# Optimization experiments

Hardware: AMD Instinct MI355X
Metric: run time of the kernel (lower is better)

## Reference

```python
import jax, jax.numpy as jnp
import numpy as np

B, C, H, W, D = 16, 512, 14, 14, 8000  # batch, channels(=input_dim1=input_dim2), spatial, output_dim


def _sketch_matrix(seed_h, seed_s, input_dim, output_dim):
    # Reproduce the module's count-sketch matrix generation (np.random.seed based).
    np.random.seed(seed_h)
    rand_h = np.random.randint(output_dim, size=input_dim)
    np.random.seed(seed_s)
    rand_s = (2 * np.random.randint(2, size=input_dim) - 1).astype(np.float32)
    M = np.zeros((input_dim, output_dim), dtype=np.float32)
    M[np.arange(input_dim), rand_h] = rand_s  # one-hot-per-row with sign
    return jnp.asarray(M)


def setup_inputs() -> dict:
    key = jax.random.key(0)
    x = jax.random.normal(key, (B, C, H, W), dtype=jnp.float32)
    S1 = _sketch_matrix(1, 3, C, D)
    S2 = _sketch_matrix(5, 7, C, D)
    return {"x": x, "S1": S1, "S2": S2}


def reference(x, S1, S2):
    b, c, h, w = x.shape
    # NCHW -> (B*H*W, C)
    flat = jnp.transpose(x, (0, 2, 3, 1)).reshape(-1, c)
    sketch1 = flat @ S1  # [BHW, D]
    sketch2 = flat @ S2  # [BHW, D]
    # circular convolution of the two count-sketches via FFT
    f1 = jnp.fft.fft(sketch1, axis=-1)
    f2 = jnp.fft.fft(sketch2, axis=-1)
    cbp_flat = jnp.fft.ifft(f1 * f2, axis=-1).real.astype(x.dtype)
    cbp = cbp_flat.reshape(b, h, w, -1)
    # sum_pool=True: reduce over spatial dims -> [B, D]
    return cbp.sum(axis=(1, 2))
```

## Files before the change

### kernel.cpp

```cpp
#include <hip/hip_runtime.h>

#define B_DIM 16
#define C_DIM 512
#define HW_DIM 196
#define D_DIM 8000
#define KP 224
#define NROW (B_DIM * C_DIM)

typedef __attribute__((ext_vector_type(8))) short short8;
typedef __attribute__((ext_vector_type(4))) float float4v;

__global__ __launch_bounds__(256) void prep(
    const float* __restrict__ x, const float* __restrict__ S1,
    const float* __restrict__ S2,
    int* __restrict__ h, float* __restrict__ s,
    unsigned short* __restrict__ xp) {
    const int bid = blockIdx.x;
    const int tid = threadIdx.x;
    if (bid < 512) {
        __shared__ int found;
        for (int rr = 0; rr < 2; ++rr) {
            const int r     = bid * 2 + rr;
            const int row   = r & (C_DIM - 1);
            const int which = r >> 9;
            const float4* rowp = (const float4*)((which ? S2 : S1) + (size_t)row * D_DIM);
            int*   hp = h + which * C_DIM;
            float* sp = s + which * C_DIM;
            if (tid == 0) found = 0;
            __syncthreads();
            for (int c = 0; c < 8; ++c) {
                int j4 = c * 256 + tid;
                if (j4 < D_DIM / 4) {
                    float4 v = rowp[j4];
                    if (v.x != 0.f) { hp[row] = 4 * j4 + 0; sp[row] = v.x; found = 1; }
                    if (v.y != 0.f) { hp[row] = 4 * j4 + 1; sp[row] = v.y; found = 1; }
                    if (v.z != 0.f) { hp[row] = 4 * j4 + 2; sp[row] = v.z; found = 1; }
                    if (v.w != 0.f) { hp[row] = 4 * j4 + 3; sp[row] = v.w; found = 1; }
                }
                __syncthreads();
                if (found) break;
            }
            __syncthreads();
        }
    } else {
        const int j = bid - 512;
        #pragma unroll
        for (int l = 0; l < 14; ++l) {
            int idx = l * 256 + tid;
            int r   = idx / KP;
            int kk  = idx - r * KP;
            int row = j * 16 + r;
            float v = (kk < HW_DIM) ? x[(size_t)row * HW_DIM + kk] : 0.0f;
            unsigned int u = __float_as_uint(v);
            u = (u + 0x7FFFu + ((u >> 16) & 1u)) >> 16;
            xp[(size_t)row * KP + kk] = (unsigned short)u;
        }
    }
}

__global__ __launch_bounds__(256) void gram_hist(
    const unsigned short* __restrict__ xp,
    const int* __restrict__ h, const float* __restrict__ s,
    float* __restrict__ part) {
    const int jb = blockIdx.x;
    const int ib = blockIdx.y;
    const int b  = blockIdx.z;
    const int i0 = ib * 128;
    const int j0 = jb * 64;
    const int tid = threadIdx.x;

    __shared__ __align__(16) float hist[D_DIM];

    #pragma unroll
    for (int l4 = 0; l4 < 7; ++l4)
        ((float4*)hist)[l4 * 256 + tid] = (float4){0.f, 0.f, 0.f, 0.f};
    if (tid < 2000 - 1792)
        ((float4*)hist)[1792 + tid] = (float4){0.f, 0.f, 0.f, 0.f};
    __syncthreads();

    const int w  = tid >> 6;
    const int l  = tid & 63;
    const int rA = l & 15;
    const int g  = l >> 4;

    const unsigned short* base = xp + (size_t)b * C_DIM * KP;
    const unsigned short* pA[2];
    const unsigned short* pB[4];
    #pragma unroll
    for (int mt = 0; mt < 2; ++mt)
        pA[mt] = base + (size_t)(i0 + w * 32 + mt * 16 + rA) * KP + g * 8;
    #pragma unroll
    for (int nt = 0; nt < 4; ++nt)
        pB[nt] = base + (size_t)(j0 + nt * 16 + rA) * KP + g * 8;

    float4v acc[2][4];
    #pragma unroll
    for (int mt = 0; mt < 2; ++mt)
        #pragma unroll
        for (int nt = 0; nt < 4; ++nt)
            acc[mt][nt] = (float4v){0.0f, 0.0f, 0.0f, 0.0f};

    short8 fa[2], fb[4];
    #pragma unroll
    for (int mt = 0; mt < 2; ++mt) fa[mt] = *(const short8*)pA[mt];
    #pragma unroll
    for (int nt = 0; nt < 4; ++nt) fb[nt] = *(const short8*)pB[nt];

    #pragma unroll
    for (int step = 1; step <= 7; ++step) {
        short8 na[2], nb[4];
        if (step < 7) {
            #pragma unroll
            for (int mt = 0; mt < 2; ++mt) na[mt] = *(const short8*)(pA[mt] + step * 32);
            #pragma unroll
            for (int nt = 0; nt < 4; ++nt) nb[nt] = *(const short8*)(pB[nt] + step * 32);
        }
        #pragma unroll
        for (int mt = 0; mt < 2; ++mt)
            #pragma unroll
            for (int nt = 0; nt < 4; ++nt)
                acc[mt][nt] = __builtin_amdgcn_mfma_f32_16x16x32_bf16(
                    fa[mt], fb[nt], acc[mt][nt], 0, 0, 0);
        if (step < 7) {
            #pragma unroll
            for (int mt = 0; mt < 2; ++mt) fa[mt] = na[mt];
            #pragma unroll
            for (int nt = 0; nt < 4; ++nt) fb[nt] = nb[nt];
        }
    }

    int hr[2][4]; float sr[2][4]; int hc[4]; float sc[4];
    #pragma unroll
    for (int mt = 0; mt < 2; ++mt)
        #pragma unroll
        for (int rg = 0; rg < 4; ++rg) {
            int c1 = i0 + w * 32 + mt * 16 + (l >> 4) * 4 + rg;
            hr[mt][rg] = h[c1]; sr[mt][rg] = s[c1];
        }
    #pragma unroll
    for (int nt = 0; nt < 4; ++nt) {
        int c2 = j0 + nt * 16 + (l & 15);
        hc[nt] = h[C_DIM + c2]; sc[nt] = s[C_DIM + c2];
    }
    #pragma unroll
    for (int mt = 0; mt < 2; ++mt)
        #pragma unroll
        for (int nt = 0; nt < 4; ++nt)
            #pragma unroll
            for (int rg = 0; rg < 4; ++rg) {
                int bin = hr[mt][rg] + hc[nt];
                if (bin >= D_DIM) bin -= D_DIM;
                atomicAdd(&hist[bin], sr[mt][rg] * sc[nt] * acc[mt][nt][rg]);
            }
    __syncthreads();

    const int slot = b * 32 + ib * 8 + jb;
    float* pb = part + (size_t)slot * D_DIM;
    #pragma unroll
    for (int l4 = 0; l4 < 7; ++l4)
        ((float4*)pb)[l4 * 256 + tid] = ((const float4*)hist)[l4 * 256 + tid];
    if (tid < 2000 - 1792)
        ((float4*)pb)[1792 + tid] = ((const float4*)hist)[1792 + tid];
}

__global__ __launch_bounds__(256) void reduce_part(
    const float* __restrict__ part, float* __restrict__ out) {
    int i4 = blockIdx.x * 256 + threadIdx.x;
    if (i4 >= B_DIM * D_DIM / 4) return;
    int b = i4 / (D_DIM / 4);
    int d = i4 - b * (D_DIM / 4);
    const float4* p = (const float4*)(part + (size_t)b * 32 * D_DIM) + d;
    float4 v = {0.f, 0.f, 0.f, 0.f};
    #pragma unroll
    for (int t = 0; t < 32; ++t) {
        float4 q = p[(size_t)t * (D_DIM / 4)];
        v.x += q.x; v.y += q.y; v.z += q.z; v.w += q.w;
    }
    ((float4*)out)[i4] = v;
}

extern "C" void kernel_launch(void* const* d_in, const int* in_sizes, int n_in,
                              void* d_out, int out_size, void* d_ws, size_t ws_size,
                              hipStream_t stream) {
    const float* x  = (const float*)d_in[0];
    const float* S1 = (const float*)d_in[1];
    const float* S2 = (const float*)d_in[2];
    float* out = (float*)d_out;

    int*            h    = (int*)d_ws;
    float*          s    = (float*)(h + 2 * C_DIM);
    unsigned short* xp   = (unsigned short*)(s + 2 * C_DIM);
    float*          part = (float*)(xp + (size_t)NROW * KP);

    prep<<<1024, 256, 0, stream>>>(x, S1, S2, h, s, xp);

    dim3 grid(8, 4, B_DIM);
    gram_hist<<<grid, 256, 0, stream>>>(xp, h, s, part);

    reduce_part<<<(B_DIM * D_DIM / 4 + 255) / 256, 256, 0, stream>>>(part, out);
}
```

Measured before the change: 117.1 us.

## Merge gram tiles into larger blocks and drop the partial-reduction kernel

Each gram_hist block now has 1024 threads and covers one quarter of a batch's rows, with every wave handling two output tiles. All tiles of a block share one LDS histogram, so there are 4 partial histograms per batch instead of 32. Those are atomically added straight into the output, which prep now zeroes, and the separate reduce kernel and its partial buffer go away. This cuts the partial-buffer memory traffic and one launch, but leaves only 64 blocks, which may underuse the GPU's compute units. It also adds global float atomics, so the summation order is no longer deterministic.

Result: slower. 177.5 us (+51.6%).

```diff
diff --git a/kernel.cpp b/kernel.cpp
--- a/kernel.cpp
+++ b/kernel.cpp
@@ -14,7 +14,7 @@
     const float* __restrict__ x, const float* __restrict__ S1,
     const float* __restrict__ S2,
     int* __restrict__ h, float* __restrict__ s,
-    unsigned short* __restrict__ xp) {
+    unsigned short* __restrict__ xp, float* __restrict__ out) {
     const int bid = blockIdx.x;
     const int tid = threadIdx.x;
     if (bid < 512) {
@@ -44,6 +44,8 @@
         }
     } else {
         const int j = bid - 512;
+        if (j < 125)
+            ((float4*)out)[j * 256 + tid] = (float4){0.f, 0.f, 0.f, 0.f};
         #pragma unroll
         for (int l = 0; l < 14; ++l) {
             int idx = l * 256 + tid;
@@ -58,24 +60,21 @@
     }
 }
 
-__global__ __launch_bounds__(256) void gram_hist(
+__global__ __launch_bounds__(1024, 4) void gram_hist(
     const unsigned short* __restrict__ xp,
     const int* __restrict__ h, const float* __restrict__ s,
-    float* __restrict__ part) {
-    const int jb = blockIdx.x;
-    const int ib = blockIdx.y;
-    const int b  = blockIdx.z;
-    const int i0 = ib * 128;
-    const int j0 = jb * 64;
+    float* __restrict__ out) {
+    const int b = blockIdx.x >> 2;
+    const int q = blockIdx.x & 3;
     const int tid = threadIdx.x;
 
     __shared__ __align__(16) float hist[D_DIM];
-
     #pragma unroll
-    for (int l4 = 0; l4 < 7; ++l4)
-        ((float4*)hist)[l4 * 256 + tid] = (float4){0.f, 0.f, 0.f, 0.f};
-    if (tid < 2000 - 1792)
-        ((float4*)hist)[1792 + tid] = (float4){0.f, 0.f, 0.f, 0.f};
+    for (int l4 = 0; l4 < 2; ++l4) {
+        int i4 = l4 * 1024 + tid;
+        if (i4 < D_DIM / 4)
+            ((float4*)hist)[i4] = (float4){0.f, 0.f, 0.f, 0.f};
+    }
     __syncthreads();
 
     const int w  = tid >> 6;
@@ -84,99 +83,92 @@
     const int g  = l >> 4;
 
     const unsigned short* base = xp + (size_t)b * C_DIM * KP;
-    const unsigned short* pA[2];
-    const unsigned short* pB[4];
+
     #pragma unroll
-    for (int mt = 0; mt < 2; ++mt)
-        pA[mt] = base + (size_t)(i0 + w * 32 + mt * 16 + rA) * KP + g * 8;
-    #pragma unroll
-    for (int nt = 0; nt < 4; ++nt)
-        pB[nt] = base + (size_t)(j0 + nt * 16 + rA) * KP + g * 8;
+    for (int pass = 0; pass < 2; ++pass) {
+        const int t  = w + pass * 16;
+        const int it = t & 3;
+        const int jt = t >> 2;
+        const int i0 = q * 128 + it * 32;
+        const int j0 = jt * 64;
 
-    float4v acc[2][4];
-    #pragma unroll
-    for (int mt = 0; mt < 2; ++mt)
+        const unsigned short* pA[2];
+        const unsigned short* pB[4];
+        #pragma unroll
+        for (int mt = 0; mt < 2; ++mt)
+            pA[mt] = base + (size_t)(i0 + mt * 16 + rA) * KP + g * 8;
         #pragma unroll
         for (int nt = 0; nt < 4; ++nt)
-            acc[mt][nt] = (float4v){0.0f, 0.0f, 0.0f, 0.0f};
+            pB[nt] = base + (size_t)(j0 + nt * 16 + rA) * KP + g * 8;
 
-    short8 fa[2], fb[4];
-    #pragma unroll
-    for (int mt = 0; mt < 2; ++mt) fa[mt] = *(const short8*)pA[mt];
-    #pragma unroll
-    for (int nt = 0; nt < 4; ++nt) fb[nt] = *(const short8*)pB[nt];
+        float4v acc[2][4];
+        #pragma unroll
+        for (int mt = 0; mt < 2; ++mt)
+            #pragma unroll
+            for (int nt = 0; nt < 4; ++nt)
+                acc[mt][nt] = (float4v){0.0f, 0.0f, 0.0f, 0.0f};
 
-    #pragma unroll
-    for (int step = 1; step <= 7; ++step) {
-        short8 na[2], nb[4];
-        if (step < 7) {
+        short8 fa[2], fb[4];
+        #pragma unroll
+        for (int mt = 0; mt < 2; ++mt) fa[mt] = *(const short8*)pA[mt];
+        #pragma unroll
+        for (int nt = 0; nt < 4; ++nt) fb[nt] = *(const short8*)pB[nt];
+
+        #pragma unroll
+        for (int step = 1; step <= 7; ++step) {
+            short8 na[2], nb[4];
+            if (step < 7) {
+                #pragma unroll
+                for (int mt = 0; mt < 2; ++mt) na[mt] = *(const short8*)(pA[mt] + step * 32);
+                #pragma unroll
+                for (int nt = 0; nt < 4; ++nt) nb[nt] = *(const short8*)(pB[nt] + step * 32);
+            }
             #pragma unroll
-            for (int mt = 0; mt < 2; ++mt) na[mt] = *(const short8*)(pA[mt] + step * 32);
+            for (int mt = 0; mt < 2; ++mt)
+                #pragma unroll
+                for (int nt = 0; nt < 4; ++nt)
+                    acc[mt][nt] = __builtin_amdgcn_mfma_f32_16x16x32_bf16(
+                        fa[mt], fb[nt], acc[mt][nt], 0, 0, 0);
+            if (step < 7) {
+                #pragma unroll
+                for (int mt = 0; mt < 2; ++mt) fa[mt] = na[mt];
+                #pragma unroll
+                for (int nt = 0; nt < 4; ++nt) fb[nt] = nb[nt];
+            }
+        }
+
+        int hr[2][4]; float sr[2][4]; int hc[4]; float sc[4];
+        #pragma unroll
+        for (int mt = 0; mt < 2; ++mt)
             #pragma unroll
-            for (int nt = 0; nt < 4; ++nt) nb[nt] = *(const short8*)(pB[nt] + step * 32);
+            for (int rg = 0; rg < 4; ++rg) {
+                int c1 = i0 + mt * 16 + (l >> 4) * 4 + rg;
+                hr[mt][rg] = h[c1]; sr[mt][rg] = s[c1];
+            }
+        #pragma unroll
+        for (int nt = 0; nt < 4; ++nt) {
+            int c2 = j0 + nt * 16 + (l & 15);
+            hc[nt] = h[C_DIM + c2]; sc[nt] = s[C_DIM + c2];
         }
         #pragma unroll
         for (int mt = 0; mt < 2; ++mt)
             #pragma unroll
             for (int nt = 0; nt < 4; ++nt)
-                acc[mt][nt] = __builtin_amdgcn_mfma_f32_16x16x32_bf16(
-                    fa[mt], fb[nt], acc[mt][nt], 0, 0, 0);
-        if (step < 7) {
-            #pragma unroll
-            for (int mt = 0; mt < 2; ++mt) fa[mt] = na[mt];
-            #pragma unroll
-            for (int nt = 0; nt < 4; ++nt) fb[nt] = nb[nt];
-        }
+                #pragma unroll
+                for (int rg = 0; rg < 4; ++rg) {
+                    int bin = hr[mt][rg] + hc[nt];
+                    if (bin >= D_DIM) bin -= D_DIM;
+                    atomicAdd(&hist[bin], sr[mt][rg] * sc[nt] * acc[mt][nt][rg]);
+                }
     }
-
-    int hr[2][4]; float sr[2][4]; int hc[4]; float sc[4];
-    #pragma unroll
-    for (int mt = 0; mt < 2; ++mt)
-        #pragma unroll
-        for (int rg = 0; rg < 4; ++rg) {
-            int c1 = i0 + w * 32 + mt * 16 + (l >> 4) * 4 + rg;
-            hr[mt][rg] = h[c1]; sr[mt][rg] = s[c1];
-        }
-    #pragma unroll
-    for (int nt = 0; nt < 4; ++nt) {
-        int c2 = j0 + nt * 16 + (l & 15);
-        hc[nt] = h[C_DIM + c2]; sc[nt] = s[C_DIM + c2];
-    }
-    #pragma unroll
-    for (int mt = 0; mt < 2; ++mt)
-        #pragma unroll
-        for (int nt = 0; nt < 4; ++nt)
-            #pragma unroll
-            for (int rg = 0; rg < 4; ++rg) {
-                int bin = hr[mt][rg] + hc[nt];
-                if (bin >= D_DIM) bin -= D_DIM;
-                atomicAdd(&hist[bin], sr[mt][rg] * sc[nt] * acc[mt][nt][rg]);
-            }
     __syncthreads();
 
-    const int slot = b * 32 + ib * 8 + jb;
-    float* pb = part + (size_t)slot * D_DIM;
+    float* outb = out + (size_t)b * D_DIM;
     #pragma unroll
-    for (int l4 = 0; l4 < 7; ++l4)
-        ((float4*)pb)[l4 * 256 + tid] = ((const float4*)hist)[l4 * 256 + tid];
-    if (tid < 2000 - 1792)
-        ((float4*)pb)[1792 + tid] = ((const float4*)hist)[1792 + tid];
-}
-
-__global__ __launch_bounds__(256) void reduce_part(
-    const float* __restrict__ part, float* __restrict__ out) {
-    int i4 = blockIdx.x * 256 + threadIdx.x;
-    if (i4 >= B_DIM * D_DIM / 4) return;
-    int b = i4 / (D_DIM / 4);
-    int d = i4 - b * (D_DIM / 4);
-    const float4* p = (const float4*)(part + (size_t)b * 32 * D_DIM) + d;
-    float4 v = {0.f, 0.f, 0.f, 0.f};
-    #pragma unroll
-    for (int t = 0; t < 32; ++t) {
-        float4 q = p[(size_t)t * (D_DIM / 4)];
-        v.x += q.x; v.y += q.y; v.z += q.z; v.w += q.w;
+    for (int l4 = 0; l4 < 8; ++l4) {
+        int d = l4 * 1024 + tid;
+        if (d < D_DIM) atomicAdd(outb + d, hist[d]);
     }
-    ((float4*)out)[i4] = v;
 }
 
 extern "C" void kernel_launch(void* const* d_in, const int* in_sizes, int n_in,
@@ -187,15 +179,11 @@
     const float* S2 = (const float*)d_in[2];
     float* out = (float*)d_out;
 
-    int*            h    = (int*)d_ws;
-    float*          s    = (float*)(h + 2 * C_DIM);
-    unsigned short* xp   = (unsigned short*)(s + 2 * C_DIM);
-    float*          part = (float*)(xp + (size_t)NROW * KP);
+    int*            h  = (int*)d_ws;
+    float*          s  = (float*)(h + 2 * C_DIM);
+    unsigned short* xp = (unsigned short*)(s + 2 * C_DIM);
 
-    prep<<<1024, 256, 0, stream>>>(x, S1, S2, h, s, xp);
+    prep<<<1024, 256, 0, stream>>>(x, S1, S2, h, s, xp, out);
 
-    dim3 grid(8, 4, B_DIM);
-    gram_hist<<<grid, 256, 0, stream>>>(xp, h, s, part);
-
-    reduce_part<<<(B_DIM * D_DIM / 4 + 255) / 256, 256, 0, stream>>>(part, out);
+    gram_hist<<<64, 1024, 0, stream>>>(xp, h, s, out);
 }
```
